# Optimization experiments

Hardware: AMD Instinct MI355X
Metric: run time of the kernel (lower is better)

The kernel has to match this reference:

```python
import jax, jax.numpy as jnp
import numpy as np

H = 1024
F = 1024


def _lstm_cell(x, h, c, Wih, Whh, b):
    # PyTorch gate order: i, f, g, o
    gates = x @ Wih.T + h @ Whh.T + b
    i, f, g, o = jnp.split(gates, 4, axis=-1)
    c = jax.nn.sigmoid(f) * c + jax.nn.sigmoid(i) * jnp.tanh(g)
    h = jax.nn.sigmoid(o) * jnp.tanh(c)
    return h, c


def setup_inputs() -> dict:
    key = jax.random.key(0)
    ks = iter(jax.random.split(key, 32))
    def rn(shape, s=0.05):
        return (s * jax.random.normal(next(ks), shape)).astype(jnp.float32)
    return {
        "tsn_feat_seq": rn((4096, F), 1.0),
        "W_fe": rn((H, F)), "b_fe": rn((H,)),
        "gW_ih0": rn((4 * H, 2 * H)), "gW_ihR": rn((4, 4 * H, H)),
        "gW_hh": rn((5, 4 * H, H)), "gb_ih": rn((5, 4 * H)), "gb_hh": rn((5, 4 * H)),
        "rW_ih": rn((4 * H, 2 * H)), "rW_hh": rn((4 * H, H)),
        "rb_ih": rn((4 * H,)), "rb_hh": rn((4 * H,)),
        "Wp": rn((H, 3 * H)), "bp": rn((H,)),
        "We2a": rn((2513, H)), "be2a": rn((2513,)),
        "We2v": rn((125, H)), "be2v": rn((125,)),
        "We2n": rn((352, H)), "be2n": rn((352,)),
    }


def reference(tsn_feat_seq, W_fe, b_fe, gW_ih0, gW_ihR, gW_hh, gb_ih, gb_hh,
              rW_ih, rW_hh, rb_ih, rb_hh, Wp, bp,
              We2a, be2a, We2v, be2v, We2n, be2n):
    # feat embedding of max-pooled TSN features (batch is always 1 after max)
    fs = jnp.max(tsn_feat_seq, axis=0) @ W_fe.T + b_fe          # [H]
    cur_action = (fs @ We2a.T + be2a)[None, :]                   # [1, 2513]

    # 5-layer goal LSTM, single time step, zero initial states;
    # input = concat(feat_state, zero action_state)
    z = jnp.zeros(H, fs.dtype)
    x = jnp.concatenate([fs, z])                                 # [2H]
    h, _ = _lstm_cell(x, z, z, gW_ih0, gW_hh[0], gb_ih[0] + gb_hh[0])
    for k in range(4):
        h, _ = _lstm_cell(h, z, z, gW_ihR[k], gW_hh[k + 1], gb_ih[k + 1] + gb_hh[k + 1])
    g = h                                                        # goal_state [H]

    rb = rb_ih + rb_hh

    def expand(a_in, f_in, best_d, best_f):
        # 10 single-layer LSTM steps with FIXED input (as in the source loop)
        xin = jnp.concatenate([a_in, f_in])                      # [2H]
        def rnn_step(carry, _):
            hh, cc = carry
            hh, cc = _lstm_cell(xin, hh, cc, rW_ih, rW_hh, rb)
            return (hh, cc), hh
        _, a_js = jax.lax.scan(rnn_step, (z, z), None, length=10)   # [10, H]
        # featpredictor: relu(Linear(concat(feat, action, goal))); dropout = eval identity
        pf = jnp.concatenate([jnp.broadcast_to(f_in, (10, H)), a_js,
                              jnp.broadcast_to(g, (10, H))], axis=1)  # [10, 3H]
        nfs = jax.nn.relu(pf @ Wp.T + bp)                        # [10, H]
        # sequential greedy best-feat update defines the scores (order matters)
        def score_step(carry, nf):
            bd, bf = carry
            d = jnp.sum((nf - g) ** 2) / H
            s = bd - d
            upd = d < bd
            return (jnp.where(upd, d, bd), jnp.where(upd, nf, bf)), s
        (bd, bf), scores = jax.lax.scan(score_step, (best_d, best_f), nfs)
        return a_js, nfs, scores, bd, bf

    # expansion 1: root node (action=0, feat=fs); best_feat_state starts at fs
    bd0 = jnp.sum((fs - g) ** 2) / H
    a1, f1, s1, bd1, bf1 = expand(z, fs, bd0, fs)
    # priority queue pops lowest score -> expansion 2 from that node
    i_star = jnp.argmin(s1)
    a2in = a1[i_star]
    f2in = f1[i_star]
    a2, f2, s2, _, _ = expand(a2in, f2in, bd1, bf1)

    # chain means: exp1 chain = [root, child]; exp2 chain = [root, n2, child]
    am = jnp.concatenate([a1 / 2.0, (a2in + a2) / 3.0], axis=0)        # [20, H]
    fm = jnp.concatenate([(fs + f1) / 2.0, (fs + f2in + f2) / 3.0], axis=0)
    scores = jnp.concatenate([s1.at[i_star].set(jnp.inf), s2])          # popped node removed
    _, idx = jax.lax.top_k(-scores, 2)                                  # 2 lowest scores, ascending
    pa = am[idx]                                                        # [2, H]
    pfeat = fm[idx]                                                     # [2, H]
    pgoal = jnp.broadcast_to(g, (2, H))

    pred_actions = pa @ We2a.T + be2a                                   # [2, 2513]
    pred_verbs = pa @ We2v.T + be2v                                     # [2, 125]
    pred_nouns = pa @ We2n.T + be2n                                     # [2, 352]
    # returned feat_state is the feat of the last popped (expanded) node
    return (pred_actions, pred_verbs, pred_nouns, pfeat, pgoal, f2in[None, :], cur_action)
```

## Files before the change

### kernel.cpp

```cpp
#include <hip/hip_runtime.h>
#include <math.h>


__device__ __forceinline__ float sigf(float x) { return 1.0f / (1.0f + expf(-x)); }

__device__ __forceinline__ float wave_red(float v) {
#pragma unroll
    for (int s = 32; s; s >>= 1) v += __shfl_down(v, s, 64);
    return v;
}

__device__ __forceinline__ float dotf(const float* __restrict__ w,
                                      const float* __restrict__ x, int lane) {
    float acc = 0.f;
#pragma unroll
    for (int j = 0; j < 4; ++j) {
        float4 a = *reinterpret_cast<const float4*>(w + j * 256 + lane * 4);
        float4 b = *reinterpret_cast<const float4*>(x + j * 256 + lane * 4);
        acc += a.x * b.x + a.y * b.y + a.z * b.z + a.w * b.w;
    }
    return acc;
}

__global__ void colmax_part_k(const float* __restrict__ tsn, float* __restrict__ part) {
    int tid = threadIdx.x;
    const float4* t4 = reinterpret_cast<const float4*>(tsn);
    float4 m = make_float4(-INFINITY, -INFINITY, -INFINITY, -INFINITY);
    int r0 = blockIdx.x * 512;
    for (int r = r0; r < r0 + 512; ++r) {
        float4 v = t4[(size_t)r * 256 + tid];
        m.x = fmaxf(m.x, v.x); m.y = fmaxf(m.y, v.y);
        m.z = fmaxf(m.z, v.z); m.w = fmaxf(m.w, v.w);
    }
    reinterpret_cast<float4*>(part + (size_t)blockIdx.x * 1024)[tid] = m;
}
__global__ void colmax_fin_k(const float* __restrict__ part, float* __restrict__ maxv) {
    int c = blockIdx.x * 256 + threadIdx.x;
    float m = -INFINITY;
    for (int b = 0; b < 8; ++b) m = fmaxf(m, part[b * 1024 + c]);
    maxv[c] = m;
}

__global__ void gemv_k(const float* __restrict__ W, int ld, int nrows,
                       const float* __restrict__ xA, int offA,
                       const float* __restrict__ xB, int offB,
                       const float* __restrict__ b1,
                       const float* __restrict__ b2,
                       float* __restrict__ yF, float* __restrict__ yOut) {
    int wave = threadIdx.x >> 6, lane = threadIdx.x & 63;
    int row = blockIdx.x * 4 + wave;
    if (row >= nrows) return;
    const float* wr = W + (size_t)row * ld;
    float acc = 0.f;
    if (xA) acc += dotf(wr + offA, xA, lane);
    if (xB) acc += dotf(wr + offB, xB, lane);
    acc = wave_red(acc);
    if (lane == 0) {
        if (b1) acc += b1[row];
        if (b2) acc += b2[row];
        if (yF) yF[row] = acc;
        if (yOut) yOut[row] = acc;
    }
}

__global__ void lstm_fused_k(const float* __restrict__ W, int ld, int off,
                             const float* __restrict__ x,
                             const float* __restrict__ b1,
                             const float* __restrict__ b2,
                             const float* __restrict__ gx,
                             const float* __restrict__ cc_in,
                             float* __restrict__ cc_out,
                             float* __restrict__ h_out) {
    __shared__ float glds[4][4];
    int wave = threadIdx.x >> 6, lane = threadIdx.x & 63;
    int j0 = blockIdx.x * 4;
#pragma unroll
    for (int jj = 0; jj < 4; ++jj) {
        int row = wave * 1024 + j0 + jj;
        float acc = dotf(W + (size_t)row * ld + off, x, lane);
        acc = wave_red(acc);
        if (lane == 0) {
            if (b1) acc += b1[row];
            if (b2) acc += b2[row];
            if (gx) acc += gx[row];
            glds[wave][jj] = acc;
        }
    }
    __syncthreads();
    if (threadIdx.x < 4) {
        int jj = threadIdx.x, j = j0 + jj;
        float gi = glds[0][jj], gf = glds[1][jj], gg = glds[2][jj], go = glds[3][jj];
        float c = sigf(gi) * tanhf(gg);
        if (cc_in) c += sigf(gf) * cc_in[j];
        float h = sigf(go) * tanhf(c);
        if (cc_out) cc_out[j] = c;
        h_out[j] = h;
    }
}

__global__ void cell0_k(const float* __restrict__ gx, float* __restrict__ cc_out,
                        float* __restrict__ h_out) {
    int j = blockIdx.x * 256 + threadIdx.x;
    float gi = gx[j], gg = gx[2048 + j], go = gx[3072 + j];
    float c = sigf(gi) * tanhf(gg);
    float h = sigf(go) * tanhf(c);
    cc_out[j] = c;
    h_out[j] = h;
}

__global__ void nfs_k(const float* __restrict__ Wp, const float* __restrict__ ajs,
                      const float* __restrict__ sv, float* __restrict__ nfs) {
    int wave = threadIdx.x >> 6, lane = threadIdx.x & 63;
    int i = blockIdx.x * 4 + wave;
    const float* wr = Wp + (size_t)i * 3072 + 1024;
    float wf[16];
#pragma unroll
    for (int j = 0; j < 4; ++j) {
        float4 a = *reinterpret_cast<const float4*>(wr + j * 256 + lane * 4);
        wf[j * 4 + 0] = a.x; wf[j * 4 + 1] = a.y; wf[j * 4 + 2] = a.z; wf[j * 4 + 3] = a.w;
    }
    float acc[10];
#pragma unroll
    for (int t = 0; t < 10; ++t) acc[t] = 0.f;
#pragma unroll
    for (int t = 0; t < 10; ++t) {
        const float* a = ajs + t * 1024;
#pragma unroll
        for (int j = 0; j < 4; ++j) {
            float4 b = *reinterpret_cast<const float4*>(a + j * 256 + lane * 4);
            acc[t] += wf[j * 4 + 0] * b.x + wf[j * 4 + 1] * b.y +
                      wf[j * 4 + 2] * b.z + wf[j * 4 + 3] * b.w;
        }
    }
#pragma unroll
    for (int t = 0; t < 10; ++t) {
        float r = wave_red(acc[t]);
        if (lane == 0) nfs[t * 1024 + i] = fmaxf(sv[i] + r, 0.f);
    }
}

__global__ void scores1_k(const float* __restrict__ nfs1, const float* __restrict__ g,
                          const float* __restrict__ fs, const float* __restrict__ ajs1,
                          float* __restrict__ s1, float* __restrict__ bd1_out,
                          int* __restrict__ istar_out, float* __restrict__ a2in,
                          float* __restrict__ f2in, float* __restrict__ out_f2in) {
    __shared__ float red[256];
    __shared__ float d[11];
    __shared__ int istar_sh;
    int tid = threadIdx.x;
    for (int t = 0; t < 11; ++t) {
        const float* v = (t < 10) ? (nfs1 + t * 1024) : fs;
        float p = 0.f;
        for (int j = tid * 4; j < tid * 4 + 4; ++j) { float df = v[j] - g[j]; p += df * df; }
        red[tid] = p; __syncthreads();
        for (int s = 128; s; s >>= 1) { if (tid < s) red[tid] += red[tid + s]; __syncthreads(); }
        if (tid == 0) d[t] = red[0] * (1.0f / 1024.0f);
        __syncthreads();
    }
    if (tid == 0) {
        float bd = d[10];
        float smin = INFINITY; int im = 0;
        for (int t = 0; t < 10; ++t) {
            float s = bd - d[t];
            s1[t] = s;
            if (s < smin) { smin = s; im = t; }
            if (d[t] < bd) bd = d[t];
        }
        *bd1_out = bd; *istar_out = im; istar_sh = im;
    }
    __syncthreads();
    int im = istar_sh;
    for (int j = tid; j < 1024; j += 256) {
        float a = ajs1[im * 1024 + j], f = nfs1[im * 1024 + j];
        a2in[j] = a; f2in[j] = f; out_f2in[j] = f;
    }
}

__global__ void scores2_k(const float* __restrict__ nfs2, const float* __restrict__ g,
                          const float* __restrict__ fs, const float* __restrict__ ajs1,
                          const float* __restrict__ nfs1, const float* __restrict__ ajs2,
                          const float* __restrict__ a2in, const float* __restrict__ f2in,
                          const float* __restrict__ s1, const float* __restrict__ bd1,
                          const int* __restrict__ istar, float* __restrict__ pa,
                          float* __restrict__ out) {
    __shared__ float red[256];
    __shared__ float d[10];
    __shared__ int sel[2];
    int tid = threadIdx.x;
    for (int t = 0; t < 10; ++t) {
        const float* v = nfs2 + t * 1024;
        float p = 0.f;
        for (int j = tid * 4; j < tid * 4 + 4; ++j) { float df = v[j] - g[j]; p += df * df; }
        red[tid] = p; __syncthreads();
        for (int s = 128; s; s >>= 1) { if (tid < s) red[tid] += red[tid + s]; __syncthreads(); }
        if (tid == 0) d[t] = red[0] * (1.0f / 1024.0f);
        __syncthreads();
    }
    if (tid == 0) {
        float sc[20];
        int im = *istar;
        for (int t = 0; t < 10; ++t) sc[t] = (t == im) ? INFINITY : s1[t];
        float bd = *bd1;
        for (int t = 0; t < 10; ++t) {
            float s = bd - d[t];
            sc[10 + t] = s;
            if (d[t] < bd) bd = d[t];
        }
        int i0 = 0; float m0 = INFINITY;
        for (int t = 0; t < 20; ++t) if (sc[t] < m0) { m0 = sc[t]; i0 = t; }
        int i1 = 0; float m1 = INFINITY;
        for (int t = 0; t < 20; ++t) { if (t == i0) continue; if (sc[t] < m1) { m1 = sc[t]; i1 = t; } }
        sel[0] = i0; sel[1] = i1;
    }
    __syncthreads();
    for (int p = 0; p < 2; ++p) {
        int idx = sel[p];
        for (int j = tid; j < 1024; j += 256) {
            float av, fv;
            if (idx < 10) {
                av = ajs1[idx * 1024 + j] * 0.5f;
                fv = (fs[j] + nfs1[idx * 1024 + j]) * 0.5f;
            } else {
                int t = idx - 10;
                av = (a2in[j] + ajs2[t * 1024 + j]) * (1.0f / 3.0f);
                fv = (fs[j] + f2in[j] + nfs2[t * 1024 + j]) * (1.0f / 3.0f);
            }
            pa[p * 1024 + j] = av;
            out[5980 + p * 1024 + j] = fv;
            out[8028 + p * 1024 + j] = g[j];
        }
    }
}

__global__ void heads_k(const float* __restrict__ We2a, const float* __restrict__ be2a,
                        const float* __restrict__ We2v, const float* __restrict__ be2v,
                        const float* __restrict__ We2n, const float* __restrict__ be2n,
                        const float* __restrict__ pa, float* __restrict__ out) {
    int wave = threadIdx.x >> 6, lane = threadIdx.x & 63;
    int task = blockIdx.x * 4 + wave;
    if (task >= 5980) return;
    int p = (task < 2990) ? 0 : 1;
    int r = task - p * 2990;
    const float* W; const float* b; int outoff, rr;
    if (r < 2513)      { W = We2a; b = be2a; rr = r;        outoff = p * 2513 + rr; }
    else if (r < 2638) { W = We2v; b = be2v; rr = r - 2513; outoff = 5026 + p * 125 + rr; }
    else               { W = We2n; b = be2n; rr = r - 2638; outoff = 5276 + p * 352 + rr; }
    float acc = dotf(W + (size_t)rr * 1024, pa + p * 1024, lane);
    acc = wave_red(acc);
    if (lane == 0) out[outoff] = acc + b[rr];
}

extern "C" void kernel_launch(void* const* d_in, const int* in_sizes, int n_in,
                              void* d_out, int out_size, void* d_ws, size_t ws_size,
                              hipStream_t stream) {
    const float* tsn    = (const float*)d_in[0];
    const float* W_fe   = (const float*)d_in[1];
    const float* b_fe   = (const float*)d_in[2];
    const float* gW_ih0 = (const float*)d_in[3];
    const float* gW_ihR = (const float*)d_in[4];
    const float* gb_ih  = (const float*)d_in[6];
    const float* gb_hh  = (const float*)d_in[7];
    const float* rW_ih  = (const float*)d_in[8];
    const float* rW_hh  = (const float*)d_in[9];
    const float* rb_ih  = (const float*)d_in[10];
    const float* rb_hh  = (const float*)d_in[11];
    const float* Wp     = (const float*)d_in[12];
    const float* bp     = (const float*)d_in[13];
    const float* We2a   = (const float*)d_in[14];
    const float* be2a   = (const float*)d_in[15];
    const float* We2v   = (const float*)d_in[16];
    const float* be2v   = (const float*)d_in[17];
    const float* We2n   = (const float*)d_in[18];
    const float* be2n   = (const float*)d_in[19];
    float* out = (float*)d_out;

    float* w = (float*)d_ws;
    float* part  = w + 0;
    float* maxv  = w + 8192;
    float* fs    = w + 9216;
    float* hgA   = w + 10240;
    float* hgB   = w + 11264;
    float* gx    = w + 12288;
    float* ajs1  = w + 16384;
    float* nfs1  = w + 26624;
    float* ajs2  = w + 36864;
    float* nfs2  = w + 47104;
    float* cc0   = w + 57344;
    float* cc1   = w + 58368;
    float* sv    = w + 59392;
    float* a2in  = w + 60416;
    float* f2in  = w + 61440;
    float* pa    = w + 62464;
    float* s1    = w + 64512;
    float* bd1   = w + 64524;
    int*   istar = (int*)(w + 64528);

    colmax_part_k<<<8, 256, 0, stream>>>(tsn, part);
    colmax_fin_k<<<4, 256, 0, stream>>>(part, maxv);
    gemv_k<<<256, 256, 0, stream>>>(W_fe, 1024, 1024, maxv, 0, nullptr, 0, b_fe, nullptr, fs, nullptr);
    gemv_k<<<629, 256, 0, stream>>>(We2a, 1024, 2513, fs, 0, nullptr, 0, be2a, nullptr, nullptr, out + 11100);

    lstm_fused_k<<<256, 256, 0, stream>>>(gW_ih0, 2048, 0, fs, gb_ih, gb_hh, nullptr, nullptr, nullptr, hgA);
    lstm_fused_k<<<256, 256, 0, stream>>>(gW_ihR + (size_t)0 * 4194304, 1024, 0, hgA, gb_ih + 1 * 4096, gb_hh + 1 * 4096, nullptr, nullptr, nullptr, hgB);
    lstm_fused_k<<<256, 256, 0, stream>>>(gW_ihR + (size_t)1 * 4194304, 1024, 0, hgB, gb_ih + 2 * 4096, gb_hh + 2 * 4096, nullptr, nullptr, nullptr, hgA);
    lstm_fused_k<<<256, 256, 0, stream>>>(gW_ihR + (size_t)2 * 4194304, 1024, 0, hgA, gb_ih + 3 * 4096, gb_hh + 3 * 4096, nullptr, nullptr, nullptr, hgB);
    lstm_fused_k<<<256, 256, 0, stream>>>(gW_ihR + (size_t)3 * 4194304, 1024, 0, hgB, gb_ih + 4 * 4096, gb_hh + 4 * 4096, nullptr, nullptr, nullptr, hgA);
    float* g = hgA;

    gemv_k<<<1024, 256, 0, stream>>>(rW_ih, 2048, 4096, nullptr, 0, fs, 1024, rb_ih, rb_hh, gx, nullptr);
    cell0_k<<<4, 256, 0, stream>>>(gx, cc0, ajs1);
    for (int t = 1; t < 10; ++t) {
        float* cin = ((t - 1) & 1) ? cc1 : cc0;
        float* cout = (t & 1) ? cc1 : cc0;
        lstm_fused_k<<<256, 256, 0, stream>>>(rW_hh, 1024, 0, ajs1 + (t - 1) * 1024,
                                              nullptr, nullptr, gx, cin, cout, ajs1 + t * 1024);
    }
    gemv_k<<<256, 256, 0, stream>>>(Wp, 3072, 1024, fs, 0, g, 2048, bp, nullptr, sv, nullptr);
    nfs_k<<<256, 256, 0, stream>>>(Wp, ajs1, sv, nfs1);
    scores1_k<<<1, 256, 0, stream>>>(nfs1, g, fs, ajs1, s1, bd1, istar, a2in, f2in, out + 10076);

    gemv_k<<<1024, 256, 0, stream>>>(rW_ih, 2048, 4096, a2in, 0, f2in, 1024, rb_ih, rb_hh, gx, nullptr);
    cell0_k<<<4, 256, 0, stream>>>(gx, cc0, ajs2);
    for (int t = 1; t < 10; ++t) {
        float* cin = ((t - 1) & 1) ? cc1 : cc0;
        float* cout = (t & 1) ? cc1 : cc0;
        lstm_fused_k<<<256, 256, 0, stream>>>(rW_hh, 1024, 0, ajs2 + (t - 1) * 1024,
                                              nullptr, nullptr, gx, cin, cout, ajs2 + t * 1024);
    }
    gemv_k<<<256, 256, 0, stream>>>(Wp, 3072, 1024, f2in, 0, g, 2048, bp, nullptr, sv, nullptr);
    nfs_k<<<256, 256, 0, stream>>>(Wp, ajs2, sv, nfs2);
    scores2_k<<<1, 256, 0, stream>>>(nfs2, g, fs, ajs1, nfs1, ajs2, a2in, f2in, s1, bd1, istar, pa, out);

    heads_k<<<1495, 256, 0, stream>>>(We2a, be2a, We2v, be2v, We2n, be2n, pa, out);
}
```

Measured before the change: 499.7 us.

## Replace kernel chain with one cooperative persistent megakernel using grid syncs

Fuses all roughly 40 launches into a single cooperative kernel with 128 blocks of 1024 threads that steps through the stages using grid.sync. The recurrent weights rW_hh are kept in registers across the 20 LSTM steps, and the cell state stays in shared memory. The column max is done with encoded atomicMax, and independent GEMVs (sv, the cur_action head) are overlapped inside one phase. This removes per-launch overhead and repeated weight reloads, at the cost of grid-wide barrier latency and high register pressure at 1024 threads per block.

```diff
diff --git a/kernel.cpp b/kernel.cpp
--- a/kernel.cpp
+++ b/kernel.cpp
@@ -1,6 +1,13 @@
 #include <hip/hip_runtime.h>
+#include <hip/hip_cooperative_groups.h>
 #include <math.h>
 
+namespace cg = cooperative_groups;
+
+
+#define NB 128
+#define NT 1024
+#define NWAVE (NB * 16)
 
 __device__ __forceinline__ float sigf(float x) { return 1.0f / (1.0f + expf(-x)); }
 
@@ -8,6 +15,14 @@
 #pragma unroll
     for (int s = 32; s; s >>= 1) v += __shfl_down(v, s, 64);
     return v;
+}
+
+__device__ __forceinline__ unsigned encf(float f) {
+    unsigned u = __float_as_uint(f);
+    return (u & 0x80000000u) ? ~u : (u | 0x80000000u);
+}
+__device__ __forceinline__ float decf(unsigned e) {
+    return (e & 0x80000000u) ? __uint_as_float(e ^ 0x80000000u) : __uint_as_float(~e);
 }
 
 __device__ __forceinline__ float dotf(const float* __restrict__ w,
@@ -22,232 +37,399 @@
     return acc;
 }
 
-__global__ void colmax_part_k(const float* __restrict__ tsn, float* __restrict__ part) {
-    int tid = threadIdx.x;
-    const float4* t4 = reinterpret_cast<const float4*>(tsn);
-    float4 m = make_float4(-INFINITY, -INFINITY, -INFINITY, -INFINITY);
-    int r0 = blockIdx.x * 512;
-    for (int r = r0; r < r0 + 512; ++r) {
-        float4 v = t4[(size_t)r * 256 + tid];
-        m.x = fmaxf(m.x, v.x); m.y = fmaxf(m.y, v.y);
-        m.z = fmaxf(m.z, v.z); m.w = fmaxf(m.w, v.w);
-    }
-    reinterpret_cast<float4*>(part + (size_t)blockIdx.x * 1024)[tid] = m;
-}
-__global__ void colmax_fin_k(const float* __restrict__ part, float* __restrict__ maxv) {
-    int c = blockIdx.x * 256 + threadIdx.x;
-    float m = -INFINITY;
-    for (int b = 0; b < 8; ++b) m = fmaxf(m, part[b * 1024 + c]);
-    maxv[c] = m;
-}
-
-__global__ void gemv_k(const float* __restrict__ W, int ld, int nrows,
-                       const float* __restrict__ xA, int offA,
-                       const float* __restrict__ xB, int offB,
-                       const float* __restrict__ b1,
-                       const float* __restrict__ b2,
-                       float* __restrict__ yF, float* __restrict__ yOut) {
-    int wave = threadIdx.x >> 6, lane = threadIdx.x & 63;
-    int row = blockIdx.x * 4 + wave;
-    if (row >= nrows) return;
-    const float* wr = W + (size_t)row * ld;
-    float acc = 0.f;
-    if (xA) acc += dotf(wr + offA, xA, lane);
-    if (xB) acc += dotf(wr + offB, xB, lane);
-    acc = wave_red(acc);
-    if (lane == 0) {
-        if (b1) acc += b1[row];
-        if (b2) acc += b2[row];
-        if (yF) yF[row] = acc;
-        if (yOut) yOut[row] = acc;
-    }
-}
-
-__global__ void lstm_fused_k(const float* __restrict__ W, int ld, int off,
-                             const float* __restrict__ x,
-                             const float* __restrict__ b1,
-                             const float* __restrict__ b2,
-                             const float* __restrict__ gx,
-                             const float* __restrict__ cc_in,
-                             float* __restrict__ cc_out,
-                             float* __restrict__ h_out) {
-    __shared__ float glds[4][4];
-    int wave = threadIdx.x >> 6, lane = threadIdx.x & 63;
-    int j0 = blockIdx.x * 4;
-#pragma unroll
-    for (int jj = 0; jj < 4; ++jj) {
-        int row = wave * 1024 + j0 + jj;
-        float acc = dotf(W + (size_t)row * ld + off, x, lane);
+__device__ __forceinline__ void dot2_acc(const float* w0, const float* w1,
+                                         const float* x, int lane, float& a0, float& a1) {
+#pragma unroll
+    for (int k = 0; k < 4; ++k) {
+        float4 xv = *reinterpret_cast<const float4*>(x + k * 256 + lane * 4);
+        float4 u = *reinterpret_cast<const float4*>(w0 + k * 256 + lane * 4);
+        float4 v = *reinterpret_cast<const float4*>(w1 + k * 256 + lane * 4);
+        a0 += u.x * xv.x + u.y * xv.y + u.z * xv.z + u.w * xv.w;
+        a1 += v.x * xv.x + v.y * xv.y + v.z * xv.z + v.w * xv.w;
+    }
+}
+
+__device__ __forceinline__ void dot2_reg(const float* __restrict__ x, int lane,
+                                         const float* wr0, const float* wr1,
+                                         float& a0, float& a1) {
+#pragma unroll
+    for (int k = 0; k < 4; ++k) {
+        float4 xv = *reinterpret_cast<const float4*>(x + k * 256 + lane * 4);
+        a0 += wr0[4 * k] * xv.x + wr0[4 * k + 1] * xv.y +
+              wr0[4 * k + 2] * xv.z + wr0[4 * k + 3] * xv.w;
+        a1 += wr1[4 * k] * xv.x + wr1[4 * k + 1] * xv.y +
+              wr1[4 * k + 2] * xv.z + wr1[4 * k + 3] * xv.w;
+    }
+}
+
+__global__ void init_k(unsigned* u) { u[512 + blockIdx.x * 256 + threadIdx.x] = 0; }
+
+__global__ void __launch_bounds__(NT, 4) mega_k(
+    const float* __restrict__ tsn, const float* __restrict__ W_fe,
+    const float* __restrict__ b_fe, const float* __restrict__ gW_ih0,
+    const float* __restrict__ gW_ihR, const float* __restrict__ gb_ih,
+    const float* __restrict__ gb_hh, const float* __restrict__ rW_ih,
+    const float* __restrict__ rW_hh, const float* __restrict__ rb_ih,
+    const float* __restrict__ rb_hh, const float* __restrict__ Wp,
+    const float* __restrict__ bp, const float* __restrict__ We2a,
+    const float* __restrict__ be2a, const float* __restrict__ We2v,
+    const float* __restrict__ be2v, const float* __restrict__ We2n,
+    const float* __restrict__ be2n, float* out, float* ws) {
+
+    cg::grid_group grid = cg::this_grid();
+
+    unsigned* maxenc = (unsigned*)ws + 512;
+    float* fs   = ws + 2048;
+    float* hgA  = ws + 3072;
+    float* hgB  = ws + 4096;
+    float* sv   = ws + 5120;
+    float* a2in = ws + 6144;
+    float* f2in = ws + 7168;
+    float* pa   = ws + 8192;
+    float* ajs1 = ws + 10240;
+    float* nfs1 = ws + 20480;
+    float* ajs2 = ws + 30720;
+    float* nfs2 = ws + 40960;
+
+    __shared__ float gg[32];
+    __shared__ float cc_l[8];
+    __shared__ float sh_d[12];
+    __shared__ float sh_s1[10];
+    __shared__ float sh_bd1;
+    __shared__ int sh_istar;
+    __shared__ int sh_sel[2];
+
+    const int tid = threadIdx.x, b = blockIdx.x;
+    const int w = tid >> 6, lane = tid & 63;
+    const int g4 = w >> 2, jr = w & 3;
+    const int ridx0 = g4 * 8 + jr, ridx1 = ridx0 + 4;
+    const int row0 = (g4 << 10) + 8 * b + jr;
+    const int row1 = row0 + 4;
+    const int gw = b * 16 + w;
+
+    float wr0[16], wr1[16];
+    {
+        const float* s0 = rW_hh + (size_t)row0 * 1024;
+        const float* s1 = rW_hh + (size_t)row1 * 1024;
+#pragma unroll
+        for (int k = 0; k < 4; ++k) {
+            float4 a = *reinterpret_cast<const float4*>(s0 + k * 256 + lane * 4);
+            float4 c = *reinterpret_cast<const float4*>(s1 + k * 256 + lane * 4);
+            wr0[4 * k] = a.x; wr0[4 * k + 1] = a.y; wr0[4 * k + 2] = a.z; wr0[4 * k + 3] = a.w;
+            wr1[4 * k] = c.x; wr1[4 * k + 1] = c.y; wr1[4 * k + 2] = c.z; wr1[4 * k + 3] = c.w;
+        }
+        float m = -INFINITY;
+        const float* tcol = tsn + (size_t)(32 * b) * 1024 + tid;
+#pragma unroll 4
+        for (int r = 0; r < 32; ++r) m = fmaxf(m, tcol[(size_t)r * 1024]);
+        atomicMax(&maxenc[tid], encf(m));
+    }
+    grid.sync();
+
+    if (gw < 1024) {
+        const float* wr = W_fe + (size_t)gw * 1024;
+        float acc = 0.f;
+#pragma unroll
+        for (int k = 0; k < 4; ++k) {
+            float4 a = *reinterpret_cast<const float4*>(wr + k * 256 + lane * 4);
+            uint4 e = *reinterpret_cast<const uint4*>(maxenc + k * 256 + lane * 4);
+            acc += a.x * decf(e.x) + a.y * decf(e.y) + a.z * decf(e.z) + a.w * decf(e.w);
+        }
         acc = wave_red(acc);
+        if (lane == 0) fs[gw] = acc + b_fe[gw];
+    }
+    grid.sync();
+
+    {
+        const float* xin = fs;
+        float* hout = hgA;
+#pragma unroll 1
+        for (int L = 0; L < 5; ++L) {
+            const float *w0p, *w1p;
+            if (L == 0) {
+                w0p = gW_ih0 + (size_t)row0 * 2048;
+                w1p = gW_ih0 + (size_t)row1 * 2048;
+            } else {
+                const float* base = gW_ihR + (size_t)(L - 1) * 4096 * 1024;
+                w0p = base + (size_t)row0 * 1024;
+                w1p = base + (size_t)row1 * 1024;
+            }
+            float a0 = 0.f, a1 = 0.f;
+            dot2_acc(w0p, w1p, xin, lane, a0, a1);
+            a0 = wave_red(a0);
+            a1 = wave_red(a1);
+            if (lane == 0) {
+                gg[ridx0] = a0 + gb_ih[L * 4096 + row0] + gb_hh[L * 4096 + row0];
+                gg[ridx1] = a1 + gb_ih[L * 4096 + row1] + gb_hh[L * 4096 + row1];
+            }
+            __syncthreads();
+            if (tid < 8) {
+                float gi = gg[tid], gc = gg[16 + tid], go = gg[24 + tid];
+                float c = sigf(gi) * tanhf(gc);
+                hout[8 * b + tid] = sigf(go) * tanhf(c);
+            }
+            grid.sync();
+            xin = hout;
+            hout = (hout == hgA) ? hgB : hgA;
+        }
+    }
+    const float* gv = hgA;
+
+    float gxr0, gxr1;
+    {
+        float a0 = 0.f, a1 = 0.f;
+        dot2_acc(rW_ih + (size_t)row0 * 2048 + 1024, rW_ih + (size_t)row1 * 2048 + 1024,
+                 fs, lane, a0, a1);
+        gxr0 = wave_red(a0);
+        gxr1 = wave_red(a1);
         if (lane == 0) {
-            if (b1) acc += b1[row];
-            if (b2) acc += b2[row];
-            if (gx) acc += gx[row];
-            glds[wave][jj] = acc;
-        }
-    }
-    __syncthreads();
-    if (threadIdx.x < 4) {
-        int jj = threadIdx.x, j = j0 + jj;
-        float gi = glds[0][jj], gf = glds[1][jj], gg = glds[2][jj], go = glds[3][jj];
-        float c = sigf(gi) * tanhf(gg);
-        if (cc_in) c += sigf(gf) * cc_in[j];
-        float h = sigf(go) * tanhf(c);
-        if (cc_out) cc_out[j] = c;
-        h_out[j] = h;
-    }
-}
-
-__global__ void cell0_k(const float* __restrict__ gx, float* __restrict__ cc_out,
-                        float* __restrict__ h_out) {
-    int j = blockIdx.x * 256 + threadIdx.x;
-    float gi = gx[j], gg = gx[2048 + j], go = gx[3072 + j];
-    float c = sigf(gi) * tanhf(gg);
-    float h = sigf(go) * tanhf(c);
-    cc_out[j] = c;
-    h_out[j] = h;
-}
-
-__global__ void nfs_k(const float* __restrict__ Wp, const float* __restrict__ ajs,
-                      const float* __restrict__ sv, float* __restrict__ nfs) {
-    int wave = threadIdx.x >> 6, lane = threadIdx.x & 63;
-    int i = blockIdx.x * 4 + wave;
-    const float* wr = Wp + (size_t)i * 3072 + 1024;
-    float wf[16];
-#pragma unroll
-    for (int j = 0; j < 4; ++j) {
-        float4 a = *reinterpret_cast<const float4*>(wr + j * 256 + lane * 4);
-        wf[j * 4 + 0] = a.x; wf[j * 4 + 1] = a.y; wf[j * 4 + 2] = a.z; wf[j * 4 + 3] = a.w;
-    }
-    float acc[10];
-#pragma unroll
-    for (int t = 0; t < 10; ++t) acc[t] = 0.f;
-#pragma unroll
-    for (int t = 0; t < 10; ++t) {
-        const float* a = ajs + t * 1024;
-#pragma unroll
-        for (int j = 0; j < 4; ++j) {
-            float4 b = *reinterpret_cast<const float4*>(a + j * 256 + lane * 4);
-            acc[t] += wf[j * 4 + 0] * b.x + wf[j * 4 + 1] * b.y +
-                      wf[j * 4 + 2] * b.z + wf[j * 4 + 3] * b.w;
-        }
-    }
-#pragma unroll
-    for (int t = 0; t < 10; ++t) {
-        float r = wave_red(acc[t]);
-        if (lane == 0) nfs[t * 1024 + i] = fmaxf(sv[i] + r, 0.f);
-    }
-}
-
-__global__ void scores1_k(const float* __restrict__ nfs1, const float* __restrict__ g,
-                          const float* __restrict__ fs, const float* __restrict__ ajs1,
-                          float* __restrict__ s1, float* __restrict__ bd1_out,
-                          int* __restrict__ istar_out, float* __restrict__ a2in,
-                          float* __restrict__ f2in, float* __restrict__ out_f2in) {
-    __shared__ float red[256];
-    __shared__ float d[11];
-    __shared__ int istar_sh;
-    int tid = threadIdx.x;
-    for (int t = 0; t < 11; ++t) {
-        const float* v = (t < 10) ? (nfs1 + t * 1024) : fs;
-        float p = 0.f;
-        for (int j = tid * 4; j < tid * 4 + 4; ++j) { float df = v[j] - g[j]; p += df * df; }
-        red[tid] = p; __syncthreads();
-        for (int s = 128; s; s >>= 1) { if (tid < s) red[tid] += red[tid + s]; __syncthreads(); }
-        if (tid == 0) d[t] = red[0] * (1.0f / 1024.0f);
-        __syncthreads();
-    }
-    if (tid == 0) {
-        float bd = d[10];
-        float smin = INFINITY; int im = 0;
-        for (int t = 0; t < 10; ++t) {
-            float s = bd - d[t];
-            s1[t] = s;
-            if (s < smin) { smin = s; im = t; }
-            if (d[t] < bd) bd = d[t];
-        }
-        *bd1_out = bd; *istar_out = im; istar_sh = im;
-    }
-    __syncthreads();
-    int im = istar_sh;
-    for (int j = tid; j < 1024; j += 256) {
-        float a = ajs1[im * 1024 + j], f = nfs1[im * 1024 + j];
-        a2in[j] = a; f2in[j] = f; out_f2in[j] = f;
-    }
-}
-
-__global__ void scores2_k(const float* __restrict__ nfs2, const float* __restrict__ g,
-                          const float* __restrict__ fs, const float* __restrict__ ajs1,
-                          const float* __restrict__ nfs1, const float* __restrict__ ajs2,
-                          const float* __restrict__ a2in, const float* __restrict__ f2in,
-                          const float* __restrict__ s1, const float* __restrict__ bd1,
-                          const int* __restrict__ istar, float* __restrict__ pa,
-                          float* __restrict__ out) {
-    __shared__ float red[256];
-    __shared__ float d[10];
-    __shared__ int sel[2];
-    int tid = threadIdx.x;
-    for (int t = 0; t < 10; ++t) {
-        const float* v = nfs2 + t * 1024;
-        float p = 0.f;
-        for (int j = tid * 4; j < tid * 4 + 4; ++j) { float df = v[j] - g[j]; p += df * df; }
-        red[tid] = p; __syncthreads();
-        for (int s = 128; s; s >>= 1) { if (tid < s) red[tid] += red[tid + s]; __syncthreads(); }
-        if (tid == 0) d[t] = red[0] * (1.0f / 1024.0f);
-        __syncthreads();
-    }
-    if (tid == 0) {
-        float sc[20];
-        int im = *istar;
-        for (int t = 0; t < 10; ++t) sc[t] = (t == im) ? INFINITY : s1[t];
-        float bd = *bd1;
-        for (int t = 0; t < 10; ++t) {
-            float s = bd - d[t];
-            sc[10 + t] = s;
-            if (d[t] < bd) bd = d[t];
-        }
-        int i0 = 0; float m0 = INFINITY;
-        for (int t = 0; t < 20; ++t) if (sc[t] < m0) { m0 = sc[t]; i0 = t; }
-        int i1 = 0; float m1 = INFINITY;
-        for (int t = 0; t < 20; ++t) { if (t == i0) continue; if (sc[t] < m1) { m1 = sc[t]; i1 = t; } }
-        sel[0] = i0; sel[1] = i1;
-    }
-    __syncthreads();
-    for (int p = 0; p < 2; ++p) {
-        int idx = sel[p];
-        for (int j = tid; j < 1024; j += 256) {
+            gxr0 += rb_ih[row0] + rb_hh[row0];
+            gxr1 += rb_ih[row1] + rb_hh[row1];
+            gg[ridx0] = gxr0;
+            gg[ridx1] = gxr1;
+        }
+        __syncthreads();
+        if (tid < 8) {
+            float gi = gg[tid], gc = gg[16 + tid], go = gg[24 + tid];
+            float c = sigf(gi) * tanhf(gc);
+            cc_l[tid] = c;
+            ajs1[8 * b + tid] = sigf(go) * tanhf(c);
+        }
+        for (int task = gw; task < 1024 + 2513; task += NWAVE) {
+            if (task < 1024) {
+                float acc = dotf(Wp + (size_t)task * 3072, fs, lane) +
+                            dotf(Wp + (size_t)task * 3072 + 2048, gv, lane);
+                acc = wave_red(acc);
+                if (lane == 0) sv[task] = acc + bp[task];
+            } else {
+                int r = task - 1024;
+                float acc = dotf(We2a + (size_t)r * 1024, fs, lane);
+                acc = wave_red(acc);
+                if (lane == 0) out[11100 + r] = acc + be2a[r];
+            }
+        }
+    }
+    grid.sync();
+
+#pragma unroll 1
+    for (int t = 1; t < 10; ++t) {
+        const float* hp = ajs1 + (t - 1) * 1024;
+        float a0 = 0.f, a1 = 0.f;
+        dot2_reg(hp, lane, wr0, wr1, a0, a1);
+        a0 = wave_red(a0);
+        a1 = wave_red(a1);
+        if (lane == 0) { gg[ridx0] = a0 + gxr0; gg[ridx1] = a1 + gxr1; }
+        __syncthreads();
+        if (tid < 8) {
+            float gi = gg[tid], gf = gg[8 + tid], gc = gg[16 + tid], go = gg[24 + tid];
+            float c = sigf(gf) * cc_l[tid] + sigf(gi) * tanhf(gc);
+            cc_l[tid] = c;
+            ajs1[t * 1024 + 8 * b + tid] = sigf(go) * tanhf(c);
+        }
+        grid.sync();
+    }
+
+    {
+        const int i = gw >> 1;
+        const int t0 = (gw & 1) * 5;
+        const float* wr = Wp + (size_t)i * 3072 + 1024;
+        float wf[16];
+#pragma unroll
+        for (int k = 0; k < 4; ++k) {
+            float4 a = *reinterpret_cast<const float4*>(wr + k * 256 + lane * 4);
+            wf[4 * k] = a.x; wf[4 * k + 1] = a.y; wf[4 * k + 2] = a.z; wf[4 * k + 3] = a.w;
+        }
+#pragma unroll
+        for (int tt = 0; tt < 5; ++tt) {
+            const float* av = ajs1 + (t0 + tt) * 1024;
+            float acc = 0.f;
+#pragma unroll
+            for (int k = 0; k < 4; ++k) {
+                float4 v = *reinterpret_cast<const float4*>(av + k * 256 + lane * 4);
+                acc += wf[4 * k] * v.x + wf[4 * k + 1] * v.y + wf[4 * k + 2] * v.z +
+                       wf[4 * k + 3] * v.w;
+            }
+            acc = wave_red(acc);
+            if (lane == 0) nfs1[(t0 + tt) * 1024 + i] = fmaxf(sv[i] + acc, 0.f);
+        }
+    }
+    grid.sync();
+
+    if (b == 0) {
+        if (w < 11) {
+            const float* vv = (w < 10) ? (nfs1 + w * 1024) : fs;
+            float p = 0.f;
+#pragma unroll
+            for (int k = 0; k < 4; ++k) {
+                float4 v = *reinterpret_cast<const float4*>(vv + k * 256 + lane * 4);
+                float4 gq = *reinterpret_cast<const float4*>(gv + k * 256 + lane * 4);
+                float dx = v.x - gq.x, dy = v.y - gq.y, dz = v.z - gq.z, dw = v.w - gq.w;
+                p += dx * dx + dy * dy + dz * dz + dw * dw;
+            }
+            p = wave_red(p);
+            if (lane == 0) sh_d[w] = p * (1.0f / 1024.0f);
+        }
+        __syncthreads();
+        if (tid == 0) {
+            float bd = sh_d[10];
+            float smin = INFINITY;
+            int im = 0;
+            for (int t = 0; t < 10; ++t) {
+                float s = bd - sh_d[t];
+                sh_s1[t] = s;
+                if (s < smin) { smin = s; im = t; }
+                if (sh_d[t] < bd) bd = sh_d[t];
+            }
+            sh_bd1 = bd;
+            sh_istar = im;
+        }
+        __syncthreads();
+        {
+            int im = sh_istar;
+            float a = ajs1[im * 1024 + tid];
+            float f = nfs1[im * 1024 + tid];
+            a2in[tid] = a;
+            f2in[tid] = f;
+            out[10076 + tid] = f;
+        }
+    }
+    grid.sync();
+
+    {
+        float a0 = 0.f, a1 = 0.f;
+        dot2_acc(rW_ih + (size_t)row0 * 2048, rW_ih + (size_t)row1 * 2048, a2in, lane, a0, a1);
+        dot2_acc(rW_ih + (size_t)row0 * 2048 + 1024, rW_ih + (size_t)row1 * 2048 + 1024,
+                 f2in, lane, a0, a1);
+        gxr0 = wave_red(a0);
+        gxr1 = wave_red(a1);
+        if (lane == 0) {
+            gxr0 += rb_ih[row0] + rb_hh[row0];
+            gxr1 += rb_ih[row1] + rb_hh[row1];
+            gg[ridx0] = gxr0;
+            gg[ridx1] = gxr1;
+        }
+        __syncthreads();
+        if (tid < 8) {
+            float gi = gg[tid], gc = gg[16 + tid], go = gg[24 + tid];
+            float c = sigf(gi) * tanhf(gc);
+            cc_l[tid] = c;
+            ajs2[8 * b + tid] = sigf(go) * tanhf(c);
+        }
+        if (gw < 1024) {
+            float acc = dotf(Wp + (size_t)gw * 3072, f2in, lane) +
+                        dotf(Wp + (size_t)gw * 3072 + 2048, gv, lane);
+            acc = wave_red(acc);
+            if (lane == 0) sv[gw] = acc + bp[gw];
+        }
+    }
+    grid.sync();
+
+#pragma unroll 1
+    for (int t = 1; t < 10; ++t) {
+        const float* hp = ajs2 + (t - 1) * 1024;
+        float a0 = 0.f, a1 = 0.f;
+        dot2_reg(hp, lane, wr0, wr1, a0, a1);
+        a0 = wave_red(a0);
+        a1 = wave_red(a1);
+        if (lane == 0) { gg[ridx0] = a0 + gxr0; gg[ridx1] = a1 + gxr1; }
+        __syncthreads();
+        if (tid < 8) {
+            float gi = gg[tid], gf = gg[8 + tid], gc = gg[16 + tid], go = gg[24 + tid];
+            float c = sigf(gf) * cc_l[tid] + sigf(gi) * tanhf(gc);
+            cc_l[tid] = c;
+            ajs2[t * 1024 + 8 * b + tid] = sigf(go) * tanhf(c);
+        }
+        grid.sync();
+    }
+
+    {
+        const int i = gw >> 1;
+        const int t0 = (gw & 1) * 5;
+        const float* wr = Wp + (size_t)i * 3072 + 1024;
+        float wf[16];
+#pragma unroll
+        for (int k = 0; k < 4; ++k) {
+            float4 a = *reinterpret_cast<const float4*>(wr + k * 256 + lane * 4);
+            wf[4 * k] = a.x; wf[4 * k + 1] = a.y; wf[4 * k + 2] = a.z; wf[4 * k + 3] = a.w;
+        }
+#pragma unroll
+        for (int tt = 0; tt < 5; ++tt) {
+            const float* av = ajs2 + (t0 + tt) * 1024;
+            float acc = 0.f;
+#pragma unroll
+            for (int k = 0; k < 4; ++k) {
+                float4 v = *reinterpret_cast<const float4*>(av + k * 256 + lane * 4);
+                acc += wf[4 * k] * v.x + wf[4 * k + 1] * v.y + wf[4 * k + 2] * v.z +
+                       wf[4 * k + 3] * v.w;
+            }
+            acc = wave_red(acc);
+            if (lane == 0) nfs2[(t0 + tt) * 1024 + i] = fmaxf(sv[i] + acc, 0.f);
+        }
+    }
+    grid.sync();
+
+    if (b == 0) {
+        if (w < 10) {
+            const float* vv = nfs2 + w * 1024;
+            float p = 0.f;
+#pragma unroll
+            for (int k = 0; k < 4; ++k) {
+                float4 v = *reinterpret_cast<const float4*>(vv + k * 256 + lane * 4);
+                float4 gq = *reinterpret_cast<const float4*>(gv + k * 256 + lane * 4);
+                float dx = v.x - gq.x, dy = v.y - gq.y, dz = v.z - gq.z, dw = v.w - gq.w;
+                p += dx * dx + dy * dy + dz * dz + dw * dw;
+            }
+            p = wave_red(p);
+            if (lane == 0) sh_d[w] = p * (1.0f / 1024.0f);
+        }
+        __syncthreads();
+        if (tid == 0) {
+            float sc[20];
+            int im = sh_istar;
+            for (int t = 0; t < 10; ++t) sc[t] = (t == im) ? INFINITY : sh_s1[t];
+            float bd = sh_bd1;
+            for (int t = 0; t < 10; ++t) {
+                float s = bd - sh_d[t];
+                sc[10 + t] = s;
+                if (sh_d[t] < bd) bd = sh_d[t];
+            }
+            int i0 = 0; float m0 = INFINITY;
+            for (int t = 0; t < 20; ++t) if (sc[t] < m0) { m0 = sc[t]; i0 = t; }
+            int i1 = 0; float m1 = INFINITY;
+            for (int t = 0; t < 20; ++t) { if (t == i0) continue; if (sc[t] < m1) { m1 = sc[t]; i1 = t; } }
+            sh_sel[0] = i0; sh_sel[1] = i1;
+        }
+        __syncthreads();
+#pragma unroll
+        for (int p = 0; p < 2; ++p) {
+            int idx = sh_sel[p];
             float av, fv;
             if (idx < 10) {
-                av = ajs1[idx * 1024 + j] * 0.5f;
-                fv = (fs[j] + nfs1[idx * 1024 + j]) * 0.5f;
+                av = ajs1[idx * 1024 + tid] * 0.5f;
+                fv = (fs[tid] + nfs1[idx * 1024 + tid]) * 0.5f;
             } else {
-                int t = idx - 10;
-                av = (a2in[j] + ajs2[t * 1024 + j]) * (1.0f / 3.0f);
-                fv = (fs[j] + f2in[j] + nfs2[t * 1024 + j]) * (1.0f / 3.0f);
-            }
-            pa[p * 1024 + j] = av;
-            out[5980 + p * 1024 + j] = fv;
-            out[8028 + p * 1024 + j] = g[j];
-        }
-    }
-}
-
-__global__ void heads_k(const float* __restrict__ We2a, const float* __restrict__ be2a,
-                        const float* __restrict__ We2v, const float* __restrict__ be2v,
-                        const float* __restrict__ We2n, const float* __restrict__ be2n,
-                        const float* __restrict__ pa, float* __restrict__ out) {
-    int wave = threadIdx.x >> 6, lane = threadIdx.x & 63;
-    int task = blockIdx.x * 4 + wave;
-    if (task >= 5980) return;
-    int p = (task < 2990) ? 0 : 1;
-    int r = task - p * 2990;
-    const float* W; const float* b; int outoff, rr;
-    if (r < 2513)      { W = We2a; b = be2a; rr = r;        outoff = p * 2513 + rr; }
-    else if (r < 2638) { W = We2v; b = be2v; rr = r - 2513; outoff = 5026 + p * 125 + rr; }
-    else               { W = We2n; b = be2n; rr = r - 2638; outoff = 5276 + p * 352 + rr; }
-    float acc = dotf(W + (size_t)rr * 1024, pa + p * 1024, lane);
-    acc = wave_red(acc);
-    if (lane == 0) out[outoff] = acc + b[rr];
+                int t2 = idx - 10;
+                av = (a2in[tid] + ajs2[t2 * 1024 + tid]) * (1.0f / 3.0f);
+                fv = (fs[tid] + f2in[tid] + nfs2[t2 * 1024 + tid]) * (1.0f / 3.0f);
+            }
+            pa[p * 1024 + tid] = av;
+            out[5980 + p * 1024 + tid] = fv;
+            out[8028 + p * 1024 + tid] = gv[tid];
+        }
+    }
+    grid.sync();
+
+    for (int task = gw; task < 5980; task += NWAVE) {
+        int p = (task < 2990) ? 0 : 1;
+        int r = task - p * 2990;
+        const float* W; const float* bb; int rr, outoff;
+        if (r < 2513)      { W = We2a; bb = be2a; rr = r;        outoff = p * 2513 + rr; }
+        else if (r < 2638) { W = We2v; bb = be2v; rr = r - 2513; outoff = 5026 + p * 125 + rr; }
+        else               { W = We2n; bb = be2n; rr = r - 2638; outoff = 5276 + p * 352 + rr; }
+        float acc = dotf(W + (size_t)rr * 1024, pa + p * 1024, lane);
+        acc = wave_red(acc);
+        if (lane == 0) out[outoff] = acc + bb[rr];
+    }
 }
 
 extern "C" void kernel_launch(void* const* d_in, const int* in_sizes, int n_in,
@@ -273,63 +455,16 @@
     const float* We2n   = (const float*)d_in[18];
     const float* be2n   = (const float*)d_in[19];
     float* out = (float*)d_out;
-
-    float* w = (float*)d_ws;
-    float* part  = w + 0;
-    float* maxv  = w + 8192;
-    float* fs    = w + 9216;
-    float* hgA   = w + 10240;
-    float* hgB   = w + 11264;
-    float* gx    = w + 12288;
-    float* ajs1  = w + 16384;
-    float* nfs1  = w + 26624;
-    float* ajs2  = w + 36864;
-    float* nfs2  = w + 47104;
-    float* cc0   = w + 57344;
-    float* cc1   = w + 58368;
-    float* sv    = w + 59392;
-    float* a2in  = w + 60416;
-    float* f2in  = w + 61440;
-    float* pa    = w + 62464;
-    float* s1    = w + 64512;
-    float* bd1   = w + 64524;
-    int*   istar = (int*)(w + 64528);
-
-    colmax_part_k<<<8, 256, 0, stream>>>(tsn, part);
-    colmax_fin_k<<<4, 256, 0, stream>>>(part, maxv);
-    gemv_k<<<256, 256, 0, stream>>>(W_fe, 1024, 1024, maxv, 0, nullptr, 0, b_fe, nullptr, fs, nullptr);
-    gemv_k<<<629, 256, 0, stream>>>(We2a, 1024, 2513, fs, 0, nullptr, 0, be2a, nullptr, nullptr, out + 11100);
-
-    lstm_fused_k<<<256, 256, 0, stream>>>(gW_ih0, 2048, 0, fs, gb_ih, gb_hh, nullptr, nullptr, nullptr, hgA);
-    lstm_fused_k<<<256, 256, 0, stream>>>(gW_ihR + (size_t)0 * 4194304, 1024, 0, hgA, gb_ih + 1 * 4096, gb_hh + 1 * 4096, nullptr, nullptr, nullptr, hgB);
-    lstm_fused_k<<<256, 256, 0, stream>>>(gW_ihR + (size_t)1 * 4194304, 1024, 0, hgB, gb_ih + 2 * 4096, gb_hh + 2 * 4096, nullptr, nullptr, nullptr, hgA);
-    lstm_fused_k<<<256, 256, 0, stream>>>(gW_ihR + (size_t)2 * 4194304, 1024, 0, hgA, gb_ih + 3 * 4096, gb_hh + 3 * 4096, nullptr, nullptr, nullptr, hgB);
-    lstm_fused_k<<<256, 256, 0, stream>>>(gW_ihR + (size_t)3 * 4194304, 1024, 0, hgB, gb_ih + 4 * 4096, gb_hh + 4 * 4096, nullptr, nullptr, nullptr, hgA);
-    float* g = hgA;
-
-    gemv_k<<<1024, 256, 0, stream>>>(rW_ih, 2048, 4096, nullptr, 0, fs, 1024, rb_ih, rb_hh, gx, nullptr);
-    cell0_k<<<4, 256, 0, stream>>>(gx, cc0, ajs1);
-    for (int t = 1; t < 10; ++t) {
-        float* cin = ((t - 1) & 1) ? cc1 : cc0;
-        float* cout = (t & 1) ? cc1 : cc0;
-        lstm_fused_k<<<256, 256, 0, stream>>>(rW_hh, 1024, 0, ajs1 + (t - 1) * 1024,
-                                              nullptr, nullptr, gx, cin, cout, ajs1 + t * 1024);
-    }
-    gemv_k<<<256, 256, 0, stream>>>(Wp, 3072, 1024, fs, 0, g, 2048, bp, nullptr, sv, nullptr);
-    nfs_k<<<256, 256, 0, stream>>>(Wp, ajs1, sv, nfs1);
-    scores1_k<<<1, 256, 0, stream>>>(nfs1, g, fs, ajs1, s1, bd1, istar, a2in, f2in, out + 10076);
-
-    gemv_k<<<1024, 256, 0, stream>>>(rW_ih, 2048, 4096, a2in, 0, f2in, 1024, rb_ih, rb_hh, gx, nullptr);
-    cell0_k<<<4, 256, 0, stream>>>(gx, cc0, ajs2);
-    for (int t = 1; t < 10; ++t) {
-        float* cin = ((t - 1) & 1) ? cc1 : cc0;
-        float* cout = (t & 1) ? cc1 : cc0;
-        lstm_fused_k<<<256, 256, 0, stream>>>(rW_hh, 1024, 0, ajs2 + (t - 1) * 1024,
-                                              nullptr, nullptr, gx, cin, cout, ajs2 + t * 1024);
-    }
-    gemv_k<<<256, 256, 0, stream>>>(Wp, 3072, 1024, f2in, 0, g, 2048, bp, nullptr, sv, nullptr);
-    nfs_k<<<256, 256, 0, stream>>>(Wp, ajs2, sv, nfs2);
-    scores2_k<<<1, 256, 0, stream>>>(nfs2, g, fs, ajs1, nfs1, ajs2, a2in, f2in, s1, bd1, istar, pa, out);
-
-    heads_k<<<1495, 256, 0, stream>>>(We2a, be2a, We2v, be2v, We2n, be2n, pa, out);
-}
+    float* wsf = (float*)d_ws;
+
+    init_k<<<4, 256, 0, stream>>>((unsigned*)d_ws);
+
+    void* args[] = {
+        (void*)&tsn,  (void*)&W_fe, (void*)&b_fe,  (void*)&gW_ih0, (void*)&gW_ihR,
+        (void*)&gb_ih, (void*)&gb_hh, (void*)&rW_ih, (void*)&rW_hh, (void*)&rb_ih,
+        (void*)&rb_hh, (void*)&Wp,   (void*)&bp,    (void*)&We2a,  (void*)&be2a,
+        (void*)&We2v, (void*)&be2v,  (void*)&We2n,  (void*)&be2n,  (void*)&out,
+        (void*)&wsf
+    };
+    hipLaunchCooperativeKernel((const void*)mega_k, dim3(NB), dim3(NT), args, 0, stream);
+}
```

New measurement: 805.6 us. 1.61x slower.
